# Optimization experiments

Hardware: AMD Instinct MI355X
Metric: run time of the kernel (lower is better)

Reference implementation:

```python
import jax, jax.numpy as jnp
import numpy as np

N = 100_000      # nodes
E = 3_200_000    # edges (avg degree 32)
F_IN = 128       # in_channels
HID = 64         # hidden_channels
G = 64           # graphs in batch


def setup_inputs() -> dict:
    key = jax.random.key(0)
    k0, k1, k2, k3 = jax.random.split(key, 4)
    x = jax.random.normal(k0, (N, F_IN), jnp.float32)
    edge_index = jax.random.randint(k1, (2, E), 0, N, dtype=jnp.int32)
    # sorted graph assignment, every graph non-empty
    batch = (jnp.arange(N, dtype=jnp.int32) * G) // N
    W1 = jax.random.normal(k2, (F_IN, HID), jnp.float32) * (1.0 / np.sqrt(F_IN))
    b1 = jnp.zeros((HID,), jnp.float32)
    W2 = jax.random.normal(k3, (HID, 1), jnp.float32) * (1.0 / np.sqrt(HID))
    b2 = jnp.zeros((1,), jnp.float32)
    return {"x": x, "edge_index": edge_index, "batch": batch,
            "W1": W1, "b1": b1, "W2": W2, "b2": b2}


def gcn_layer(x, src, dst, W, b):
    """GCNConv: add self-loops, symmetric deg^-1/2 norm, scatter-add, bias."""
    h = x @ W  # transform first (smaller messages)
    loops = jnp.arange(N, dtype=src.dtype)
    s = jnp.concatenate([src, loops])
    d = jnp.concatenate([dst, loops])
    deg = jax.ops.segment_sum(jnp.ones(s.shape[0], x.dtype), d, num_segments=N)
    dinv = jnp.where(deg > 0, jax.lax.rsqrt(deg), 0.0)
    norm = dinv[s] * dinv[d]                         # [E+N]
    out = jax.ops.segment_sum(h[s] * norm[:, None], d, num_segments=N)
    return out + b


def reference(x, edge_index, batch, W1, b1, W2, b2):
    src, dst = edge_index[0], edge_index[1]
    h = jax.nn.relu(gcn_layer(x, src, dst, W1, b1))
    h = gcn_layer(h, src, dst, W2, b2)               # [N, 1]
    counts = jax.ops.segment_sum(jnp.ones(N, jnp.int32), batch, num_segments=G)
    big_node_idx = jnp.cumsum(counts) - 1            # last node of each graph
    return h[big_node_idx].squeeze(-1)               # [G]
```

## Files before the change

kernel.cpp:

```cpp
#include <hip/hip_runtime.h>

#define N_NODES 100000
#define N_EDGES 3200000
#define F_IN    128
#define HID     64
#define NGRAPH  64

#define NBUK    196
#define BSHIFT  9
#define BCAP    18432
#define CHUNK   5120
#define NBLK_A  625
#define SLICES  8
#define NWORDS  3200
#define MAXDEG  96
#define NIDCAP  4096
#define L2DEG   8
#define NBLK_X  2176


__device__ __forceinline__ bool is_big(int v, const int* __restrict__ batch) {
    return (v == N_NODES - 1) || (batch[v] != batch[v + 1]);
}
__device__ __forceinline__ float dinv_of(int degv) {
    return rsqrtf((float)(degv + 1));
}

__global__ void k_init(const int* __restrict__ batch, unsigned* __restrict__ bigmask,
                       unsigned* __restrict__ nmask, int* __restrict__ nid_of,
                       int* __restrict__ nlist, int* __restrict__ counters,
                       int* __restrict__ bcnt, int* __restrict__ incnt,
                       int* __restrict__ l2cnt, int* __restrict__ deg,
                       const float* __restrict__ b2, float* __restrict__ out) {
    const int t = threadIdx.x;
    const int bx = blockIdx.x;
    if (bx == 0) {
        if (t < 64) { counters[t] = (t == 2) ? NGRAPH : 0; out[t] = b2[0]; }
        bcnt[t] = 0;
    } else if (bx <= 16) {
        incnt[(bx - 1) * 256 + t] = 0;
    } else if (bx <= 32) {
        l2cnt[(bx - 17) * 256 + t] = 0;
    }
    int v = bx * 256 + t;
    bool big = (v < N_NODES) && is_big(v, batch);
    unsigned long long m = __ballot(big);
    if (v < N_NODES) {
        deg[v] = 0;
        int g = big ? batch[v] : -1;
        nid_of[v] = g;
        if (big) nlist[g] = v;
        int lane = t & 63;
        if (lane == 0)  { unsigned w = (unsigned)m;         bigmask[v >> 5] = w; nmask[v >> 5] = w; }
        if (lane == 32) { unsigned w = (unsigned)(m >> 32); bigmask[v >> 5] = w; nmask[v >> 5] = w; }
    }
}

__global__ __launch_bounds__(256) void k_partA(const int* __restrict__ src,
        const int* __restrict__ dst, const unsigned* __restrict__ bigmask,
        unsigned* __restrict__ nmask, int* __restrict__ nid_of,
        int* __restrict__ nlist, int* __restrict__ counters,
        unsigned* __restrict__ plist, int* __restrict__ bcnt) {
    __shared__ unsigned staged[CHUNK];
    __shared__ unsigned char sbkt[CHUNK];
    __shared__ int hist4[4][NBUK];
    __shared__ int startb[256];
    __shared__ int curb[NBUK], gbasea[NBUK];
    __shared__ int wsum[4];
    const int t = threadIdx.x;
    const int lane = t & 63;
    const int w = t >> 6;
    for (int i = t; i < NBUK; i += 256) {
        hist4[0][i] = 0; hist4[1][i] = 0; hist4[2][i] = 0; hist4[3][i] = 0;
    }
    __syncthreads();

    const int E0 = blockIdx.x * CHUNK;
    const int4* s4 = (const int4*)(src + E0);
    const int4* d4 = (const int4*)(dst + E0);
    int vloc[20]; unsigned pk[20];
#pragma unroll
    for (int it = 0; it < 5; ++it) {
        int4 dd = d4[t + it * 256];
        int4 ss = s4[t + it * 256];
        int vv[4] = {dd.x, dd.y, dd.z, dd.w};
        int uu[4] = {ss.x, ss.y, ss.z, ss.w};
#pragma unroll
        for (int j = 0; j < 4; ++j) {
            int v = vv[j], u = uu[j];
            vloc[it * 4 + j] = v;
            pk[it * 4 + j] = ((unsigned)u << BSHIFT) | (unsigned)(v & 511);
            atomicAdd(&hist4[w][v >> BSHIFT], 1);
            if ((bigmask[v >> 5] >> (v & 31)) & 1) {
                unsigned bit = 1u << (u & 31);
                unsigned old = atomicOr(&nmask[u >> 5], bit);
                if (!(old & bit)) {
                    int p = atomicAdd(&counters[2], 1);
                    if (p < NIDCAP) { nid_of[u] = p; nlist[p] = u; }
                }
            }
        }
    }
    __syncthreads();
    int c = 0;
    if (t < NBUK) c = hist4[0][t] + hist4[1][t] + hist4[2][t] + hist4[3][t];
    int sc = c;
#pragma unroll
    for (int off = 1; off < 64; off <<= 1) {
        int y = __shfl_up(sc, off, 64);
        if (lane >= off) sc += y;
    }
    if (lane == 63) wsum[w] = sc;
    __syncthreads();
    int pre = 0;
#pragma unroll
    for (int k = 0; k < 4; ++k) pre += (k < w) ? wsum[k] : 0;
    int excl = pre + sc - c;
    startb[t] = excl;
    if (t < NBUK) {
        curb[t]   = excl;
        gbasea[t] = atomicAdd(&bcnt[t], c);
    }
    __syncthreads();
#pragma unroll
    for (int it = 0; it < 20; ++it) {
        int b = vloc[it] >> BSHIFT;
        int pos = atomicAdd(&curb[b], 1);
        staged[pos] = pk[it];
        sbkt[pos]   = (unsigned char)b;
    }
    __syncthreads();
    for (int i = t; i < CHUNK; i += 256) {
        int b = sbkt[i];
        int s = gbasea[b] + (i - startb[b]);
        if (s < BCAP) plist[(size_t)b * BCAP + s] = staged[i];
    }
}

__global__ __launch_bounds__(256) void k_partB(const unsigned* __restrict__ plist,
        const int* __restrict__ bcnt, const unsigned* __restrict__ nmask,
        const unsigned* __restrict__ bigmask, const int* __restrict__ nid_of,
        int* __restrict__ incnt, int* __restrict__ csr, int* __restrict__ deg,
        int* __restrict__ l2cnt, int* __restrict__ csr2) {
    __shared__ int bins[512];
    const int b = blockIdx.x / SLICES, s = blockIdx.x % SLICES;
    for (int i = threadIdx.x; i < 512; i += 256) bins[i] = 0;
    __syncthreads();
    int n = bcnt[b]; if (n > BCAP) n = BCAP;
    const int i0 = (int)((long)n * s / SLICES);
    const int i1 = (int)((long)n * (s + 1) / SLICES);
    const unsigned* lp = plist + (size_t)b * BCAP;
    const int lo = b << BSHIFT;
    for (int i = i0 + threadIdx.x; i < i1; i += 256) {
        unsigned e = lp[i];
        int local = (int)(e & 511u);
        atomicAdd(&bins[local], 1);
        int v = lo + local;
        if ((nmask[v >> 5] >> (v & 31)) & 1) {
            int nidv = nid_of[v];
            int u = (int)(e >> BSHIFT);
            if (nidv >= 0) {
                int slot = atomicAdd(&incnt[nidv], 1);
                if (slot < MAXDEG) csr[nidv * MAXDEG + slot] = u;
            }
            if ((bigmask[v >> 5] >> (v & 31)) & 1) {
                int nidu = nid_of[u];
                if (nidu >= 0) {
                    int s2 = atomicAdd(&l2cnt[nidu], 1);
                    if (s2 < L2DEG) csr2[nidu * L2DEG + s2] = v;
                }
            }
        }
    }
    __syncthreads();
    for (int i = threadIdx.x; i < 512; i += 256) {
        int v = lo + i, c = bins[i];
        if (c > 0 && v < N_NODES) atomicAdd(&deg[v], c);
    }
}

__global__ __launch_bounds__(256) void k_xaggtrans(const int* __restrict__ nlist,
        const int* __restrict__ incnt, const int* __restrict__ csr,
        const int* __restrict__ deg, const float* __restrict__ x,
        const float* __restrict__ W1, const float* __restrict__ b1,
        const float* __restrict__ W2, const int* __restrict__ counters,
        const int* __restrict__ l2cnt, const int* __restrict__ csr2,
        const int* __restrict__ batch, float* __restrict__ out) {
    __shared__ float4 sm[8][32];
    __shared__ float xaggL[F_IN];
    __shared__ float p2[4 * HID];
    int ncnt = counters[2]; if (ncnt > NIDCAP) ncnt = NIDCAP;
    const int tid = threadIdx.x;
    const int l = tid & 31, g = tid >> 5;
    const int f = tid & 63, gg = tid >> 6;
    for (int nid = blockIdx.x; nid < ncnt; nid += gridDim.x) {
        int v = nlist[nid];
        if (v < 0) continue;
        int m = incnt[nid]; if (m > MAXDEG) m = MAXDEG;
        const int* cs = csr + nid * MAXDEG;
        float4 acc = make_float4(0.f, 0.f, 0.f, 0.f);
        for (int j = g; j < m; j += 8) {
            int u = cs[j];
            float du = dinv_of(deg[u]);
            float4 xr = ((const float4*)(x + (size_t)u * F_IN))[l];
            acc.x += du * xr.x; acc.y += du * xr.y;
            acc.z += du * xr.z; acc.w += du * xr.w;
        }
        sm[g][l] = acc;
        __syncthreads();
        if (tid < 32) {
            float4 tot = make_float4(0.f, 0.f, 0.f, 0.f);
#pragma unroll
            for (int k = 0; k < 8; ++k) {
                float4 p = sm[k][tid];
                tot.x += p.x; tot.y += p.y; tot.z += p.z; tot.w += p.w;
            }
            float dv = dinv_of(deg[v]);
            float4 xv = ((const float4*)(x + (size_t)v * F_IN))[tid];
            float4 r;
            r.x = dv * tot.x + dv * dv * xv.x;
            r.y = dv * tot.y + dv * dv * xv.y;
            r.z = dv * tot.z + dv * dv * xv.z;
            r.w = dv * tot.w + dv * dv * xv.w;
            ((float4*)xaggL)[tid] = r;
        }
        __syncthreads();
        float a = 0.f;
#pragma unroll
        for (int k0 = 0; k0 < 32; ++k0) {
            int k = gg * 32 + k0;
            a += xaggL[k] * W1[(size_t)k * HID + f];
        }
        p2[gg * HID + f] = a;
        __syncthreads();
        if (tid < HID) {
            float h = p2[tid] + p2[HID + tid] + p2[2 * HID + tid] + p2[3 * HID + tid] + b1[tid];
            float cc = fmaxf(h, 0.f) * W2[tid];
#pragma unroll
            for (int off = 32; off > 0; off >>= 1) cc += __shfl_down(cc, off, 64);
            if (tid == 0) {
                float du = dinv_of(deg[v]);
                int c2 = l2cnt[nid]; if (c2 > L2DEG) c2 = L2DEG;
                for (int j = 0; j < c2; ++j) {
                    int wv = csr2[nid * L2DEG + j];
                    atomicAdd(&out[batch[wv]], du * dinv_of(deg[wv]) * cc);
                }
                if (nid < NGRAPH)
                    atomicAdd(&out[nid], du * du * cc);
            }
        }
        __syncthreads();
    }
}

extern "C" void kernel_launch(void* const* d_in, const int* in_sizes, int n_in,
                              void* d_out, int out_size, void* d_ws, size_t ws_size,
                              hipStream_t stream) {
    const float* x     = (const float*)d_in[0];
    const int*   eidx  = (const int*)d_in[1];
    const int*   src   = eidx;
    const int*   dst   = eidx + N_EDGES;
    const int*   batch = (const int*)d_in[2];
    const float* W1    = (const float*)d_in[3];
    const float* b1    = (const float*)d_in[4];
    const float* W2    = (const float*)d_in[5];
    const float* b2    = (const float*)d_in[6];
    float*       out   = (float*)d_out;

    char* ws = (char*)d_ws;
    size_t off = 0;
    int*      counters = (int*)(ws + off);      off += 256;
    int*      bcnt     = (int*)(ws + off);      off += 1024;
    unsigned* nmask    = (unsigned*)(ws + off); off += NWORDS * 4;
    unsigned* bigmask  = (unsigned*)(ws + off); off += NWORDS * 4;
    int*      incnt    = (int*)(ws + off);      off += NIDCAP * 4;
    int*      l2cnt    = (int*)(ws + off);      off += NIDCAP * 4;
    int*      deg      = (int*)(ws + off);      off += (size_t)N_NODES * 4;
    int*      nid_of   = (int*)(ws + off);      off += (size_t)N_NODES * 4;
    int*      nlist    = (int*)(ws + off);      off += (size_t)NIDCAP * 4;
    int*      csr2     = (int*)(ws + off);      off += (size_t)NIDCAP * L2DEG * 4;
    int*      csr      = (int*)(ws + off);      off += (size_t)NIDCAP * MAXDEG * 4;
    unsigned* plist    = (unsigned*)(ws + off); off += (size_t)NBUK * BCAP * 4;
    if (off > ws_size) return;

    const int BN = (N_NODES + 255) / 256;

    k_init<<<BN, 256, 0, stream>>>(batch, bigmask, nmask, nid_of, nlist, counters,
                                   bcnt, incnt, l2cnt, deg, b2, out);
    k_partA<<<NBLK_A, 256, 0, stream>>>(src, dst, bigmask, nmask, nid_of, nlist,
                                        counters, plist, bcnt);
    k_partB<<<NBUK * SLICES, 256, 0, stream>>>(plist, bcnt, nmask, bigmask, nid_of,
                                               incnt, csr, deg, l2cnt, csr2);
    k_xaggtrans<<<NBLK_X, 256, 0, stream>>>(nlist, incnt, csr, deg, x, W1, b1, W2,
                                            counters, l2cnt, csr2, batch, out);
}
```

Baseline: 185.0 us.

## Replace bucketed edge partitioning with two direct edge scans using global atomics

Drops the two-stage radix-bucket partition (shared-memory histogram, staging, and a plist write then re-read). Instead, two plain scans read the edge arrays directly. The first scan counts degrees with global atomics and marks neighbors of big nodes. The second builds the small CSR lists for marked nodes. This removes the plist write/read traffic and the shared-memory scan, at the cost of 3.2M scattered global atomicAdds on deg and a second full read of dst, while src is read only for relevant edges.

```diff
diff --git a/kernel.cpp b/kernel.cpp
--- a/kernel.cpp
+++ b/kernel.cpp
@@ -6,17 +6,12 @@
 #define HID     64
 #define NGRAPH  64
 
-#define NBUK    196
-#define BSHIFT  9
-#define BCAP    18432
-#define CHUNK   5120
-#define NBLK_A  625
-#define SLICES  8
 #define NWORDS  3200
 #define MAXDEG  96
 #define NIDCAP  4096
 #define L2DEG   8
 #define NBLK_X  2176
+#define NBLK_S  3125
 
 
 __device__ __forceinline__ bool is_big(int v, const int* __restrict__ batch) {
@@ -29,14 +24,13 @@
 __global__ void k_init(const int* __restrict__ batch, unsigned* __restrict__ bigmask,
                        unsigned* __restrict__ nmask, int* __restrict__ nid_of,
                        int* __restrict__ nlist, int* __restrict__ counters,
-                       int* __restrict__ bcnt, int* __restrict__ incnt,
-                       int* __restrict__ l2cnt, int* __restrict__ deg,
+                       int* __restrict__ incnt, int* __restrict__ l2cnt,
+                       int* __restrict__ deg,
                        const float* __restrict__ b2, float* __restrict__ out) {
     const int t = threadIdx.x;
     const int bx = blockIdx.x;
     if (bx == 0) {
         if (t < 64) { counters[t] = (t == 2) ? NGRAPH : 0; out[t] = b2[0]; }
-        bcnt[t] = 0;
     } else if (bx <= 16) {
         incnt[(bx - 1) * 256 + t] = 0;
     } else if (bx <= 32) {
@@ -56,109 +50,44 @@
     }
 }
 
-__global__ __launch_bounds__(256) void k_partA(const int* __restrict__ src,
+__global__ __launch_bounds__(256) void k_scan1(const int* __restrict__ src,
         const int* __restrict__ dst, const unsigned* __restrict__ bigmask,
         unsigned* __restrict__ nmask, int* __restrict__ nid_of,
         int* __restrict__ nlist, int* __restrict__ counters,
-        unsigned* __restrict__ plist, int* __restrict__ bcnt) {
-    __shared__ unsigned staged[CHUNK];
-    __shared__ unsigned char sbkt[CHUNK];
-    __shared__ int hist4[4][NBUK];
-    __shared__ int startb[256];
-    __shared__ int curb[NBUK], gbasea[NBUK];
-    __shared__ int wsum[4];
-    const int t = threadIdx.x;
-    const int lane = t & 63;
-    const int w = t >> 6;
-    for (int i = t; i < NBUK; i += 256) {
-        hist4[0][i] = 0; hist4[1][i] = 0; hist4[2][i] = 0; hist4[3][i] = 0;
-    }
-    __syncthreads();
-
-    const int E0 = blockIdx.x * CHUNK;
-    const int4* s4 = (const int4*)(src + E0);
-    const int4* d4 = (const int4*)(dst + E0);
-    int vloc[20]; unsigned pk[20];
-#pragma unroll
-    for (int it = 0; it < 5; ++it) {
-        int4 dd = d4[t + it * 256];
-        int4 ss = s4[t + it * 256];
-        int vv[4] = {dd.x, dd.y, dd.z, dd.w};
-        int uu[4] = {ss.x, ss.y, ss.z, ss.w};
-#pragma unroll
-        for (int j = 0; j < 4; ++j) {
-            int v = vv[j], u = uu[j];
-            vloc[it * 4 + j] = v;
-            pk[it * 4 + j] = ((unsigned)u << BSHIFT) | (unsigned)(v & 511);
-            atomicAdd(&hist4[w][v >> BSHIFT], 1);
-            if ((bigmask[v >> 5] >> (v & 31)) & 1) {
-                unsigned bit = 1u << (u & 31);
-                unsigned old = atomicOr(&nmask[u >> 5], bit);
-                if (!(old & bit)) {
-                    int p = atomicAdd(&counters[2], 1);
-                    if (p < NIDCAP) { nid_of[u] = p; nlist[p] = u; }
-                }
-            }
-        }
-    }
-    __syncthreads();
-    int c = 0;
-    if (t < NBUK) c = hist4[0][t] + hist4[1][t] + hist4[2][t] + hist4[3][t];
-    int sc = c;
-#pragma unroll
-    for (int off = 1; off < 64; off <<= 1) {
-        int y = __shfl_up(sc, off, 64);
-        if (lane >= off) sc += y;
-    }
-    if (lane == 63) wsum[w] = sc;
-    __syncthreads();
-    int pre = 0;
-#pragma unroll
-    for (int k = 0; k < 4; ++k) pre += (k < w) ? wsum[k] : 0;
-    int excl = pre + sc - c;
-    startb[t] = excl;
-    if (t < NBUK) {
-        curb[t]   = excl;
-        gbasea[t] = atomicAdd(&bcnt[t], c);
-    }
-    __syncthreads();
-#pragma unroll
-    for (int it = 0; it < 20; ++it) {
-        int b = vloc[it] >> BSHIFT;
-        int pos = atomicAdd(&curb[b], 1);
-        staged[pos] = pk[it];
-        sbkt[pos]   = (unsigned char)b;
-    }
-    __syncthreads();
-    for (int i = t; i < CHUNK; i += 256) {
-        int b = sbkt[i];
-        int s = gbasea[b] + (i - startb[b]);
-        if (s < BCAP) plist[(size_t)b * BCAP + s] = staged[i];
-    }
-}
-
-__global__ __launch_bounds__(256) void k_partB(const unsigned* __restrict__ plist,
-        const int* __restrict__ bcnt, const unsigned* __restrict__ nmask,
+        int* __restrict__ deg) {
+    const int i4 = blockIdx.x * 256 + threadIdx.x;
+    const int4 dd = ((const int4*)dst)[i4];
+    int vv[4] = {dd.x, dd.y, dd.z, dd.w};
+#pragma unroll
+    for (int j = 0; j < 4; ++j) {
+        int v = vv[j];
+        atomicAdd(&deg[v], 1);
+        if ((bigmask[v >> 5] >> (v & 31)) & 1) {
+            int u = src[i4 * 4 + j];
+            unsigned bit = 1u << (u & 31);
+            unsigned old = atomicOr(&nmask[u >> 5], bit);
+            if (!(old & bit)) {
+                int p = atomicAdd(&counters[2], 1);
+                if (p < NIDCAP) { nid_of[u] = p; nlist[p] = u; }
+            }
+        }
+    }
+}
+
+__global__ __launch_bounds__(256) void k_scan2(const int* __restrict__ src,
+        const int* __restrict__ dst, const unsigned* __restrict__ nmask,
         const unsigned* __restrict__ bigmask, const int* __restrict__ nid_of,
-        int* __restrict__ incnt, int* __restrict__ csr, int* __restrict__ deg,
+        int* __restrict__ incnt, int* __restrict__ csr,
         int* __restrict__ l2cnt, int* __restrict__ csr2) {
-    __shared__ int bins[512];
-    const int b = blockIdx.x / SLICES, s = blockIdx.x % SLICES;
-    for (int i = threadIdx.x; i < 512; i += 256) bins[i] = 0;
-    __syncthreads();
-    int n = bcnt[b]; if (n > BCAP) n = BCAP;
-    const int i0 = (int)((long)n * s / SLICES);
-    const int i1 = (int)((long)n * (s + 1) / SLICES);
-    const unsigned* lp = plist + (size_t)b * BCAP;
-    const int lo = b << BSHIFT;
-    for (int i = i0 + threadIdx.x; i < i1; i += 256) {
-        unsigned e = lp[i];
-        int local = (int)(e & 511u);
-        atomicAdd(&bins[local], 1);
-        int v = lo + local;
+    const int i4 = blockIdx.x * 256 + threadIdx.x;
+    const int4 dd = ((const int4*)dst)[i4];
+    int vv[4] = {dd.x, dd.y, dd.z, dd.w};
+#pragma unroll
+    for (int j = 0; j < 4; ++j) {
+        int v = vv[j];
         if ((nmask[v >> 5] >> (v & 31)) & 1) {
+            int u = src[i4 * 4 + j];
             int nidv = nid_of[v];
-            int u = (int)(e >> BSHIFT);
             if (nidv >= 0) {
                 int slot = atomicAdd(&incnt[nidv], 1);
                 if (slot < MAXDEG) csr[nidv * MAXDEG + slot] = u;
@@ -171,11 +100,6 @@
                 }
             }
         }
-    }
-    __syncthreads();
-    for (int i = threadIdx.x; i < 512; i += 256) {
-        int v = lo + i, c = bins[i];
-        if (c > 0 && v < N_NODES) atomicAdd(&deg[v], c);
     }
 }
 
@@ -270,7 +194,6 @@
     char* ws = (char*)d_ws;
     size_t off = 0;
     int*      counters = (int*)(ws + off);      off += 256;
-    int*      bcnt     = (int*)(ws + off);      off += 1024;
     unsigned* nmask    = (unsigned*)(ws + off); off += NWORDS * 4;
     unsigned* bigmask  = (unsigned*)(ws + off); off += NWORDS * 4;
     int*      incnt    = (int*)(ws + off);      off += NIDCAP * 4;
@@ -280,17 +203,16 @@
     int*      nlist    = (int*)(ws + off);      off += (size_t)NIDCAP * 4;
     int*      csr2     = (int*)(ws + off);      off += (size_t)NIDCAP * L2DEG * 4;
     int*      csr      = (int*)(ws + off);      off += (size_t)NIDCAP * MAXDEG * 4;
-    unsigned* plist    = (unsigned*)(ws + off); off += (size_t)NBUK * BCAP * 4;
     if (off > ws_size) return;
 
     const int BN = (N_NODES + 255) / 256;
 
     k_init<<<BN, 256, 0, stream>>>(batch, bigmask, nmask, nid_of, nlist, counters,
-                                   bcnt, incnt, l2cnt, deg, b2, out);
-    k_partA<<<NBLK_A, 256, 0, stream>>>(src, dst, bigmask, nmask, nid_of, nlist,
-                                        counters, plist, bcnt);
-    k_partB<<<NBUK * SLICES, 256, 0, stream>>>(plist, bcnt, nmask, bigmask, nid_of,
-                                               incnt, csr, deg, l2cnt, csr2);
+                                   incnt, l2cnt, deg, b2, out);
+    k_scan1<<<NBLK_S, 256, 0, stream>>>(src, dst, bigmask, nmask, nid_of, nlist,
+                                        counters, deg);
+    k_scan2<<<NBLK_S, 256, 0, stream>>>(src, dst, nmask, bigmask, nid_of,
+                                        incnt, csr, l2cnt, csr2);
     k_xaggtrans<<<NBLK_X, 256, 0, stream>>>(nlist, incnt, csr, deg, x, W1, b1, W2,
                                             counters, l2cnt, csr2, batch, out);
 }
```

Measured after the change: 276.7 us. +49.6%, slower.
